# Optimization experiments

Hardware: AMD Instinct MI355X
Metric: run time of the kernel (lower is better)

The kernel has to match this reference:

```python
import jax, jax.numpy as jnp
import numpy as np

IN_C, H1, H2, FC1, NCLS = 16, 32, 64, 128, 10
N_NODES, N_EDGES = 20000, 100000


def _glorot(key, shape):
    fan_in, fan_out = shape[0], shape[-1]
    s = jnp.sqrt(6.0 / (fan_in + fan_out))
    return jax.random.uniform(key, shape, jnp.float32, -s, s)


def setup_inputs() -> dict:
    key = jax.random.key(0)
    ks = jax.random.split(key, 20)
    x = jax.random.normal(ks[0], (N_NODES, IN_C), jnp.float32)
    edge_index = jax.random.randint(ks[1], (2, N_EDGES), 0, N_NODES, jnp.int64)
    edge_attr = jax.random.uniform(ks[2], (N_EDGES, 1), jnp.float32)
    return {
        "x": x,
        "edge_index": edge_index,
        "edge_attr": edge_attr,
        # conv1 edge-MLP: 1 -> 25 -> IN_C*H1
        "w1a": _glorot(ks[3], (1, 25)), "b1a": jnp.zeros((25,), jnp.float32),
        "w1b": _glorot(ks[4], (25, IN_C * H1)), "b1b": jnp.zeros((IN_C * H1,), jnp.float32),
        "wr1": _glorot(ks[5], (IN_C, H1)), "bias1": jnp.zeros((H1,), jnp.float32),
        # conv2 edge-MLP: 1 -> 25 -> H1*H2 (=2048)
        "w2a": _glorot(ks[6], (1, 25)), "b2a": jnp.zeros((25,), jnp.float32),
        "w2b": _glorot(ks[7], (25, H1 * H2)), "b2b": jnp.zeros((H1 * H2,), jnp.float32),
        "wr2": _glorot(ks[8], (H1, H2)), "bias2": jnp.zeros((H2,), jnp.float32),
        # trailing FCs
        "fc1_w": _glorot(ks[9], (H2, FC1)), "fc1_b": jnp.zeros((FC1,), jnp.float32),
        "fc2_w": _glorot(ks[10], (FC1, NCLS)), "fc2_b": jnp.zeros((NCLS,), jnp.float32),
    }


def _nnconv(x, src, tgt, edge_attr, wa, ba, wb, bb, wroot, bias, in_c, out_c):
    # per-edge MLP-generated weight matrix [E, in_c, out_c]
    h = jax.nn.relu(edge_attr @ wa + ba) @ wb + bb
    W = h.reshape(-1, in_c, out_c)
    # gather source feats, per-edge matmul, scatter-max to targets
    msg = jnp.einsum("ei,eio->eo", x[src], W)  # [E, out_c]
    agg = jax.ops.segment_max(msg, tgt, num_segments=x.shape[0])
    agg = jnp.where(jnp.isfinite(agg), agg, 0.0)  # nodes with no in-edges -> 0 (PyG behavior)
    return agg + x @ wroot + bias


def reference(x, edge_index, edge_attr,
              w1a, b1a, w1b, b1b, wr1, bias1,
              w2a, b2a, w2b, b2b, wr2, bias2,
              fc1_w, fc1_b, fc2_w, fc2_b):
    src, tgt = edge_index[0], edge_index[1]
    h = jax.nn.elu(_nnconv(x, src, tgt, edge_attr, w1a, b1a, w1b, b1b, wr1, bias1, IN_C, H1))
    h = jax.nn.elu(_nnconv(h, src, tgt, edge_attr, w2a, b2a, w2b, b2b, wr2, bias2, H1, H2))
    h = jax.nn.elu(h @ fc1_w + fc1_b)
    h = h @ fc2_w + fc2_b
    return jax.nn.log_softmax(h, axis=1)
```

## Files before the change

kernel.cpp:

```cpp
#include <hip/hip_runtime.h>
#include <float.h>
#include <math.h>


#define NCONST 25
#define CH1 32
#define CH2 16
#define PACK_MASK 0x1FFFF
#define TNB 4

__device__ __forceinline__ void atomicMaxFloat(float* addr, float val) {
    if (val >= 0.f) atomicMax((int*)addr, __float_as_int(val));
    else            atomicMin((unsigned int*)addr, __float_as_uint(val));
}
__device__ __forceinline__ float readlane_f(float v, int l) {
    return __int_as_float(__builtin_amdgcn_readlane(__float_as_int(v), l));
}
__device__ __forceinline__ float elu_f(float a) {
    return a > 0.f ? a : expm1f(a);
}

__global__ void fill_kernel(float* agg, int nAgg, int* ords, int nOrd, int* hist, int nH) {
    int i = blockIdx.x * blockDim.x + threadIdx.x;
    int stride = gridDim.x * blockDim.x;
    int total = nAgg + nOrd + nH;
    for (; i < total; i += stride) {
        if (i < nAgg) agg[i] = -FLT_MAX;
        else if (i < nAgg + nOrd) ords[i - nAgg] = -1;
        else hist[i - nAgg - nOrd] = 0;
    }
}

__global__ void assign_hist_kernel(const float* __restrict__ ea,
                                   const float* __restrict__ w1a, const float* __restrict__ b1a,
                                   const float* __restrict__ w2a, const float* __restrict__ b2a,
                                   int E, int* __restrict__ segpack, int* __restrict__ hist) {
    __shared__ float t1[NCONST], t2[NCONST];
    __shared__ int lh[64];
    int tid = threadIdx.x;
    if (tid < NCONST) {
        float w = w1a[tid]; t1[tid] = (w != 0.f) ? (-b1a[tid] / w) : INFINITY;
        float v = w2a[tid]; t2[tid] = (v != 0.f) ? (-b2a[tid] / v) : INFINITY;
    }
    if (tid < 64) lh[tid] = 0;
    __syncthreads();
    int e = blockIdx.x * blockDim.x + tid;
    bool valid = e < E;
    if (valid) {
        float a = ea[e];
        int j1 = 0, j2 = 0;
        for (int k = 0; k < NCONST; ++k) { j1 += (t1[k] < a); j2 += (t2[k] < a); }
        segpack[e] = j1 | (j2 << 8);
        atomicAdd(&lh[j1], 1); atomicAdd(&lh[32 + j2], 1);
    }
    __syncthreads();
    if (tid < 64 && lh[tid]) atomicAdd(&hist[tid], lh[tid]);
}

__global__ void scanpad_kernel(const int* __restrict__ hist, int* __restrict__ cur) {
    __shared__ int h[64];
    int tid = threadIdx.x;
    h[tid] = hist[tid];
    __syncthreads();
    if (tid == 0) {
        int off = 0;
        for (int j = 0; j < 26; ++j) { cur[j] = off; off += ((h[j] + CH1 - 1) / CH1) * CH1; }
    } else if (tid == 1) {
        int off = 0;
        for (int j = 0; j < 26; ++j) { cur[32 + j] = off; off += ((h[32 + j] + CH2 - 1) / CH2) * CH2; }
    }
}

__global__ void scatter_kernel(const int* __restrict__ segpack, int E, int* __restrict__ cur,
                               int* __restrict__ order1, int* __restrict__ order2) {
    __shared__ int lh[64], lb[64];
    int tid = threadIdx.x;
    if (tid < 64) lh[tid] = 0;
    __syncthreads();
    int e = blockIdx.x * blockDim.x + tid;
    bool valid = e < E;
    int j1 = 0, j2 = 0, r1 = 0, r2 = 0;
    if (valid) {
        int p = segpack[e]; j1 = p & 0xFF; j2 = p >> 8;
        r1 = atomicAdd(&lh[j1], 1); r2 = atomicAdd(&lh[32 + j2], 1);
    }
    __syncthreads();
    if (tid < 64 && lh[tid]) lb[tid] = atomicAdd(&cur[tid], lh[tid]);
    __syncthreads();
    if (valid) {
        order1[lb[j1] + r1] = (j1 << 17) | e;
        order2[lb[32 + j2] + r2] = (j2 << 17) | e;
    }
}

__global__ void build_uv_fused(const float* w1a, const float* b1a, const float* w1b, const float* b1b,
                               const float* w2a, const float* b2a, const float* w2b, const float* b2b,
                               float* U1, float* V1, float* U2, float* V2) {
    __shared__ float swa[NCONST], sba[NCONST], st[NCONST];
    __shared__ int sr[NCONST];
    __shared__ unsigned msk_sh;
    int seg = blockIdx.y;
    int bx = blockIdx.x;
    int conv = (bx < 2) ? 0 : 1;
    const float* wa = conv ? w2a : w1a;
    const float* ba = conv ? b2a : b1a;
    int tid = threadIdx.x;
    if (tid < NCONST) {
        float w = wa[tid], b = ba[tid];
        swa[tid] = w; sba[tid] = b;
        st[tid] = (w != 0.f) ? (-b / w) : INFINITY;
    }
    __syncthreads();
    if (tid < NCONST) {
        int rk = 0;
        for (int l = 0; l < NCONST; ++l) rk += (st[l] < st[tid]) ? 1 : 0;
        sr[tid] = rk;
    }
    __syncthreads();
    if (tid == 0) {
        unsigned m = 0;
        for (int k = 0; k < NCONST; ++k) {
            float w = swa[k];
            bool act = (w > 0.f) ? (seg > sr[k])
                     : (w < 0.f) ? (seg <= sr[k])
                                 : (sba[k] > 0.f);
            if (act) m |= (1u << k);
        }
        msk_sh = m;
    }
    __syncthreads();
    unsigned msk = msk_sh;
    if (conv == 0) {
        int idx = bx * 256 + tid;
        float u = 0.f, v = 0.f;
        for (int k = 0; k < NCONST; ++k)
            if (msk & (1u << k)) { float w = w1b[k * 512 + idx]; u = fmaf(swa[k], w, u); v = fmaf(sba[k], w, v); }
        v += b1b[idx];
        U1[seg * 512 + idx] = u; V1[seg * 512 + idx] = v;
    } else {
        int idx = (bx - 2) * 256 + tid;
        float u = 0.f, v = 0.f;
        for (int k = 0; k < NCONST; ++k)
            if (msk & (1u << k)) { float w = w2b[k * 2048 + idx]; u = fmaf(swa[k], w, u); v = fmaf(sba[k], w, v); }
        v += b2b[idx];
        U2[seg * 2048 + idx] = u; V2[seg * 2048 + idx] = v;
    }
}

__global__ void edge1_kernel(const float* __restrict__ xin, const int* __restrict__ src,
                             const int* __restrict__ tgt, const float* __restrict__ ea,
                             const int* __restrict__ order, int cap,
                             const float* __restrict__ U, const float* __restrict__ V,
                             float* __restrict__ agg) {
    int wid = (blockIdx.x * blockDim.x + threadIdx.x) >> 6;
    int lane = threadIdx.x & 63;
    int base = wid * CH1;
    if (base >= cap) return;
    int pk = order[base + (lane & (CH1 - 1))];
    int p0 = __builtin_amdgcn_readfirstlane(pk);
    if (p0 < 0) return;
    int seg = p0 >> 17;
    int ev = (pk < 0) ? 0 : (pk & PACK_MASK);
    int sv = src[ev], tv = tgt[ev];
    float av = ea[ev];
    int half = lane >> 5, c = lane & 31;
    float Ur[16], Vr[16];
    {
        const float* Us = U + seg * 512 + c;
        const float* Vs = V + seg * 512 + c;
#pragma unroll
        for (int i = 0; i < 16; ++i) { Ur[i] = Us[i * 32]; Vr[i] = Vs[i * 32]; }
    }
#pragma unroll
    for (int t = 0; t < CH1; t += 2) {
        int pA = __builtin_amdgcn_readlane(pk, t);
        int pB = __builtin_amdgcn_readlane(pk, t + 1);
        int sA = __builtin_amdgcn_readlane(sv, t);
        int sB = __builtin_amdgcn_readlane(sv, t + 1);
        int tA = __builtin_amdgcn_readlane(tv, t);
        int tB = __builtin_amdgcn_readlane(tv, t + 1);
        float aA = readlane_f(av, t);
        float aB = readlane_f(av, t + 1);
        const float* xA = xin + sA * 16;
        const float* xB = xin + sB * 16;
        float ah = half ? aB : aA;
        int   th = half ? tB : tA;
        int   ph = half ? pB : pA;
        float acc = 0.f;
#pragma unroll
        for (int i = 0; i < 16; ++i) {
            float xi = half ? xB[i] : xA[i];
            acc = fmaf(xi, fmaf(ah, Ur[i], Vr[i]), acc);
        }
        if (ph >= 0) atomicMaxFloat(&agg[th * 32 + c], acc);
    }
}

__global__ void edge2_kernel(const float* __restrict__ xin, const int* __restrict__ src,
                             const int* __restrict__ tgt, const float* __restrict__ ea,
                             const int* __restrict__ order, int cap,
                             const float* __restrict__ U, const float* __restrict__ V,
                             float* __restrict__ agg) {
    int wid = (blockIdx.x * blockDim.x + threadIdx.x) >> 6;
    int lane = threadIdx.x & 63;
    int base = wid * CH2;
    if (base >= cap) return;
    int pk = order[base + (lane & (CH2 - 1))];
    int p0 = __builtin_amdgcn_readfirstlane(pk);
    if (p0 < 0) return;
    int seg = p0 >> 17;
    int ev = (pk < 0) ? 0 : (pk & PACK_MASK);
    int sv = src[ev], tv = tgt[ev];
    float av = ea[ev];
    float Ur[32], Vr[32];
    {
        const float* Us = U + seg * 2048 + lane;
        const float* Vs = V + seg * 2048 + lane;
#pragma unroll
        for (int i = 0; i < 32; ++i) { Ur[i] = Us[i * 64]; Vr[i] = Vs[i * 64]; }
    }
#pragma unroll
    for (int t = 0; t < CH2; t += 2) {
        int pA = __builtin_amdgcn_readlane(pk, t);
        int pB = __builtin_amdgcn_readlane(pk, t + 1);
        int sA = __builtin_amdgcn_readlane(sv, t);
        int sB = __builtin_amdgcn_readlane(sv, t + 1);
        int tA = __builtin_amdgcn_readlane(tv, t);
        int tB = __builtin_amdgcn_readlane(tv, t + 1);
        float aA = readlane_f(av, t);
        float aB = readlane_f(av, t + 1);
        const float* xA = xin + sA * 32;
        const float* xB = xin + sB * 32;
        float accA = 0.f, accB = 0.f;
#pragma unroll
        for (int i = 0; i < 32; ++i) {
            accA = fmaf(xA[i], fmaf(aA, Ur[i], Vr[i]), accA);
            accB = fmaf(xB[i], fmaf(aB, Ur[i], Vr[i]), accB);
        }
        if (pA >= 0) atomicMaxFloat(&agg[tA * 64 + lane], accA);
        if (pB >= 0) atomicMaxFloat(&agg[tB * 64 + lane], accB);
    }
}

__global__ void node1_kernel(const float* __restrict__ xin, const float* __restrict__ agg,
                             const float* __restrict__ wroot, const float* __restrict__ bias,
                             float* __restrict__ out, int N) {
    int idx = blockIdx.x * blockDim.x + threadIdx.x;
    if (idx >= N * 32) return;
    int n = idx >> 5, c = idx & 31;
    float v = agg[idx];
    if (v == -FLT_MAX) v = 0.f;
    float acc = v + bias[c];
#pragma unroll
    for (int i = 0; i < 16; ++i) acc = fmaf(xin[n * 16 + i], wroot[i * 32 + c], acc);
    out[idx] = acc > 0.f ? acc : expm1f(acc);
}

__global__ void tail_kernel(const float* __restrict__ h1, const float* __restrict__ agg2,
                            const float* __restrict__ wr2, const float* __restrict__ bias2,
                            const float* __restrict__ fc1w, const float* __restrict__ fc1b,
                            const float* __restrict__ fc2w, const float* __restrict__ fc2b,
                            float* __restrict__ out) {
    __shared__ __align__(16) float h1sh[4][TNB][32];
    __shared__ __align__(16) float h2sh[4][TNB][64];
    __shared__ __align__(16) float h3sh[4][TNB][132];
    __shared__ __align__(16) float wTsh[10][132];
    int tid = threadIdx.x;
    int wv = tid >> 6, lane = tid & 63;

    for (int t = tid; t < 1280; t += 256) {
        int k = t / 10, j = t - k * 10;
        wTsh[j][k] = fc2w[t];
    }
    __syncthreads();

    int nb = blockIdx.x * (4 * TNB) + wv * TNB;

    {
        const float2* hp = (const float2*)(h1 + (size_t)nb * 32);
        ((float2*)&h1sh[wv][0][0])[lane] = hp[lane];
    }

    float b2v = bias2[lane];
    float ac0 = agg2[(size_t)(nb + 0) * 64 + lane];
    float ac1 = agg2[(size_t)(nb + 1) * 64 + lane];
    float ac2 = agg2[(size_t)(nb + 2) * 64 + lane];
    float ac3 = agg2[(size_t)(nb + 3) * 64 + lane];
    ac0 = (ac0 == -FLT_MAX ? 0.f : ac0) + b2v;
    ac1 = (ac1 == -FLT_MAX ? 0.f : ac1) + b2v;
    ac2 = (ac2 == -FLT_MAX ? 0.f : ac2) + b2v;
    ac3 = (ac3 == -FLT_MAX ? 0.f : ac3) + b2v;
#pragma unroll 8
    for (int i = 0; i < 32; ++i) {
        float w = wr2[i * 64 + lane];
        ac0 = fmaf(h1sh[wv][0][i], w, ac0);
        ac1 = fmaf(h1sh[wv][1][i], w, ac1);
        ac2 = fmaf(h1sh[wv][2][i], w, ac2);
        ac3 = fmaf(h1sh[wv][3][i], w, ac3);
    }
    h2sh[wv][0][lane] = elu_f(ac0);
    h2sh[wv][1][lane] = elu_f(ac1);
    h2sh[wv][2][lane] = elu_f(ac2);
    h2sh[wv][3][lane] = elu_f(ac3);

    float fb1 = fc1b[lane], fb2 = fc1b[64 + lane];
    float p0 = fb1, p1 = fb1, p2 = fb1, p3 = fb1;
    float q0 = fb2, q1 = fb2, q2 = fb2, q3 = fb2;
#pragma unroll 2
    for (int k4 = 0; k4 < 16; ++k4) {
        int k = k4 * 4;
        float wA0 = fc1w[(k + 0) * 128 + lane];
        float wB0 = fc1w[(k + 0) * 128 + 64 + lane];
        float wA1 = fc1w[(k + 1) * 128 + lane];
        float wB1 = fc1w[(k + 1) * 128 + 64 + lane];
        float wA2 = fc1w[(k + 2) * 128 + lane];
        float wB2 = fc1w[(k + 2) * 128 + 64 + lane];
        float wA3 = fc1w[(k + 3) * 128 + lane];
        float wB3 = fc1w[(k + 3) * 128 + 64 + lane];
        float4 g0 = ((const float4*)h2sh[wv][0])[k4];
        float4 g1 = ((const float4*)h2sh[wv][1])[k4];
        float4 g2 = ((const float4*)h2sh[wv][2])[k4];
        float4 g3 = ((const float4*)h2sh[wv][3])[k4];
        p0 = fmaf(g0.x, wA0, p0); p0 = fmaf(g0.y, wA1, p0);
        p0 = fmaf(g0.z, wA2, p0); p0 = fmaf(g0.w, wA3, p0);
        q0 = fmaf(g0.x, wB0, q0); q0 = fmaf(g0.y, wB1, q0);
        q0 = fmaf(g0.z, wB2, q0); q0 = fmaf(g0.w, wB3, q0);
        p1 = fmaf(g1.x, wA0, p1); p1 = fmaf(g1.y, wA1, p1);
        p1 = fmaf(g1.z, wA2, p1); p1 = fmaf(g1.w, wA3, p1);
        q1 = fmaf(g1.x, wB0, q1); q1 = fmaf(g1.y, wB1, q1);
        q1 = fmaf(g1.z, wB2, q1); q1 = fmaf(g1.w, wB3, q1);
        p2 = fmaf(g2.x, wA0, p2); p2 = fmaf(g2.y, wA1, p2);
        p2 = fmaf(g2.z, wA2, p2); p2 = fmaf(g2.w, wA3, p2);
        q2 = fmaf(g2.x, wB0, q2); q2 = fmaf(g2.y, wB1, q2);
        q2 = fmaf(g2.z, wB2, q2); q2 = fmaf(g2.w, wB3, q2);
        p3 = fmaf(g3.x, wA0, p3); p3 = fmaf(g3.y, wA1, p3);
        p3 = fmaf(g3.z, wA2, p3); p3 = fmaf(g3.w, wA3, p3);
        q3 = fmaf(g3.x, wB0, q3); q3 = fmaf(g3.y, wB1, q3);
        q3 = fmaf(g3.z, wB2, q3); q3 = fmaf(g3.w, wB3, q3);
    }
    h3sh[wv][0][lane] = elu_f(p0); h3sh[wv][0][64 + lane] = elu_f(q0);
    h3sh[wv][1][lane] = elu_f(p1); h3sh[wv][1][64 + lane] = elu_f(q1);
    h3sh[wv][2][lane] = elu_f(p2); h3sh[wv][2][64 + lane] = elu_f(q2);
    h3sh[wv][3][lane] = elu_f(p3); h3sh[wv][3][64 + lane] = elu_f(q3);

    {
        int n = lane >> 4, j = lane & 15;
        bool act = j < 10;
        int jc = act ? j : 0;
        float a = fc2b[jc];
        const float4* h3v = (const float4*)h3sh[wv][n];
        const float4* wv4 = (const float4*)wTsh[jc];
#pragma unroll
        for (int q = 0; q < 32; ++q) {
            float4 h = h3v[q];
            float4 w = wv4[q];
            a = fmaf(h.x, w.x, a);
            a = fmaf(h.y, w.y, a);
            a = fmaf(h.z, w.z, a);
            a = fmaf(h.w, w.w, a);
        }
        float lm = act ? a : -FLT_MAX;
        lm = fmaxf(lm, __shfl_xor(lm, 1, 16));
        lm = fmaxf(lm, __shfl_xor(lm, 2, 16));
        lm = fmaxf(lm, __shfl_xor(lm, 4, 16));
        lm = fmaxf(lm, __shfl_xor(lm, 8, 16));
        float ls = act ? expf(a - lm) : 0.f;
        ls += __shfl_xor(ls, 1, 16);
        ls += __shfl_xor(ls, 2, 16);
        ls += __shfl_xor(ls, 4, 16);
        ls += __shfl_xor(ls, 8, 16);
        if (act) out[(size_t)(nb + n) * 10 + j] = a - lm - logf(ls);
    }
}

extern "C" void kernel_launch(void* const* d_in, const int* in_sizes, int n_in,
                              void* d_out, int out_size, void* d_ws, size_t ws_size,
                              hipStream_t stream) {
    const float* x     = (const float*)d_in[0];
    const int*   eidx  = (const int*)d_in[1];
    const float* ea    = (const float*)d_in[2];
    const float* w1a   = (const float*)d_in[3];
    const float* b1a   = (const float*)d_in[4];
    const float* w1b   = (const float*)d_in[5];
    const float* b1b   = (const float*)d_in[6];
    const float* wr1   = (const float*)d_in[7];
    const float* bias1 = (const float*)d_in[8];
    const float* w2a   = (const float*)d_in[9];
    const float* b2a   = (const float*)d_in[10];
    const float* w2b   = (const float*)d_in[11];
    const float* b2b   = (const float*)d_in[12];
    const float* wr2   = (const float*)d_in[13];
    const float* bias2 = (const float*)d_in[14];
    const float* fc1w  = (const float*)d_in[15];
    const float* fc1b  = (const float*)d_in[16];
    const float* fc2w  = (const float*)d_in[17];
    const float* fc2b  = (const float*)d_in[18];

    const int N = in_sizes[0] / 16;
    const int E = in_sizes[2];
    const int* src = eidx;
    const int* tgt = eidx + E;

    const int cap1 = ((E + 26 * (CH1 - 1)) + CH1 - 1) / CH1 * CH1;
    const int cap2 = ((E + 26 * (CH2 - 1)) + CH2 - 1) / CH2 * CH2;

    float* ws = (float*)d_ws;
    size_t off = 0;
    int*      hist = (int*)(ws + off);      off += 64;
    int*      cur  = (int*)(ws + off);      off += 64;
    int*      segp = (int*)(ws + off);      off += E;
    int*      ord1 = (int*)(ws + off);      off += cap1;
    int*      ord2 = (int*)(ws + off);      off += cap2;
    float*    U1   = ws + off;              off += 26 * 512;
    float*    V1   = ws + off;              off += 26 * 512;
    float*    U2   = ws + off;              off += 26 * 2048;
    float*    V2   = ws + off;              off += 26 * 2048;
    float*    AGG1 = ws + off;              off += (size_t)N * 32;
    float*    AGG2 = ws + off;              off += (size_t)N * 64;
    float*    H1b  = ws + off;              off += (size_t)N * 32;

    fill_kernel<<<512, 256, 0, stream>>>(AGG1, N * 96, ord1, cap1 + cap2, hist, 64);
    assign_hist_kernel<<<(E + 255) / 256, 256, 0, stream>>>(ea, w1a, b1a, w2a, b2a, E, segp, hist);
    scanpad_kernel<<<1, 64, 0, stream>>>(hist, cur);
    scatter_kernel<<<(E + 255) / 256, 256, 0, stream>>>(segp, E, cur, ord1, ord2);
    build_uv_fused<<<dim3(10, 26), 256, 0, stream>>>(w1a, b1a, w1b, b1b, w2a, b2a, w2b, b2b,
                                                     U1, V1, U2, V2);
    {
        int waves = cap1 / CH1;
        edge1_kernel<<<(waves + 3) / 4, 256, 0, stream>>>(x, src, tgt, ea, ord1, cap1, U1, V1, AGG1);
    }
    node1_kernel<<<(N * 32 + 255) / 256, 256, 0, stream>>>(x, AGG1, wr1, bias1, H1b, N);
    {
        int waves = cap2 / CH2;
        edge2_kernel<<<(waves + 3) / 4, 256, 0, stream>>>(H1b, src, tgt, ea, ord2, cap2, U2, V2, AGG2);
    }
    tail_kernel<<<N / 16, 256, 0, stream>>>(H1b, AGG2, wr2, bias2, fc1w, fc1b, fc2w, fc2b, (float*)d_out);
}
```

Before: 198.2 us.

## Merge fill, UV build and histogram into one prep kernel; fold scan into scatter

```diff
diff --git a/kernel.cpp b/kernel.cpp
--- a/kernel.cpp
+++ b/kernel.cpp
@@ -8,6 +8,8 @@
 #define CH2 16
 #define PACK_MASK 0x1FFFF
 #define TNB 4
+#define K1_FILL 512
+#define K1_UV   260
 
 __device__ __forceinline__ void atomicMaxFloat(float* addr, float val) {
     if (val >= 0.f) atomicMax((int*)addr, __float_as_int(val));
@@ -20,154 +22,145 @@
     return a > 0.f ? a : expm1f(a);
 }
 
-__global__ void fill_kernel(float* agg, int nAgg, int* ords, int nOrd, int* hist, int nH) {
-    int i = blockIdx.x * blockDim.x + threadIdx.x;
-    int stride = gridDim.x * blockDim.x;
-    int total = nAgg + nOrd + nH;
-    for (; i < total; i += stride) {
-        if (i < nAgg) agg[i] = -FLT_MAX;
-        else if (i < nAgg + nOrd) ords[i - nAgg] = -1;
-        else hist[i - nAgg - nOrd] = 0;
-    }
-}
-
-__global__ void assign_hist_kernel(const float* __restrict__ ea,
-                                   const float* __restrict__ w1a, const float* __restrict__ b1a,
-                                   const float* __restrict__ w2a, const float* __restrict__ b2a,
-                                   int E, int* __restrict__ segpack, int* __restrict__ hist) {
+struct Params {
+    const float *x; const int *src; const int *tgt; const float *ea;
+    const float *w1a, *b1a, *w1b, *b1b, *wr1, *bias1;
+    const float *w2a, *b2a, *w2b, *b2b, *wr2, *bias2;
+    const float *fc1w, *fc1b, *fc2w, *fc2b;
+    float *out;
+    int *hist, *cur, *segp, *ord1, *ord2;
+    float *U1, *V1, *U2, *V2, *AGG1, *AGG2, *H1b;
+    int N, E, cap1, cap2;
+};
+
+__global__ void prep_kernel(Params p) {
     __shared__ float t1[NCONST], t2[NCONST];
     __shared__ int lh[64];
+    __shared__ float swa[NCONST], sba[NCONST], stt[NCONST];
+    __shared__ int srk[NCONST];
+    __shared__ unsigned msk_sh;
+    const int bid = blockIdx.x, tid = threadIdx.x;
+
+    if (bid < K1_FILL) {
+        int nAgg = p.N * 96, total = nAgg + p.cap1 + p.cap2;
+        for (int i = bid * 256 + tid; i < total; i += K1_FILL * 256) {
+            if (i < nAgg) p.AGG1[i] = -FLT_MAX;
+            else p.ord1[i - nAgg] = -1;
+        }
+    } else if (bid < K1_FILL + K1_UV) {
+        int v = bid - K1_FILL;
+        int seg = v / 10;
+        int bx  = v % 10;
+        int conv = (bx < 2) ? 0 : 1;
+        const float* wa = conv ? p.w2a : p.w1a;
+        const float* ba = conv ? p.b2a : p.b1a;
+        if (tid < NCONST) {
+            float w = wa[tid], b = ba[tid];
+            swa[tid] = w; sba[tid] = b;
+            stt[tid] = (w != 0.f) ? (-b / w) : INFINITY;
+        }
+        __syncthreads();
+        if (tid < NCONST) {
+            int rk = 0;
+            for (int l = 0; l < NCONST; ++l) rk += (stt[l] < stt[tid]) ? 1 : 0;
+            srk[tid] = rk;
+        }
+        __syncthreads();
+        if (tid == 0) {
+            unsigned m = 0;
+            for (int k = 0; k < NCONST; ++k) {
+                float w = swa[k];
+                bool act = (w > 0.f) ? (seg > srk[k])
+                         : (w < 0.f) ? (seg <= srk[k])
+                                     : (sba[k] > 0.f);
+                if (act) m |= (1u << k);
+            }
+            msk_sh = m;
+        }
+        __syncthreads();
+        unsigned msk = msk_sh;
+        if (conv == 0) {
+            int idx = bx * 256 + tid;
+            float u = 0.f, vv = 0.f;
+            for (int k = 0; k < NCONST; ++k)
+                if (msk & (1u << k)) { float w = p.w1b[k * 512 + idx]; u = fmaf(swa[k], w, u); vv = fmaf(sba[k], w, vv); }
+            vv += p.b1b[idx];
+            p.U1[seg * 512 + idx] = u; p.V1[seg * 512 + idx] = vv;
+        } else {
+            int idx = (bx - 2) * 256 + tid;
+            float u = 0.f, vv = 0.f;
+            for (int k = 0; k < NCONST; ++k)
+                if (msk & (1u << k)) { float w = p.w2b[k * 2048 + idx]; u = fmaf(swa[k], w, u); vv = fmaf(sba[k], w, vv); }
+            vv += p.b2b[idx];
+            p.U2[seg * 2048 + idx] = u; p.V2[seg * 2048 + idx] = vv;
+        }
+    } else {
+        if (tid < NCONST) {
+            float w = p.w1a[tid]; t1[tid] = (w != 0.f) ? (-p.b1a[tid] / w) : INFINITY;
+            float v = p.w2a[tid]; t2[tid] = (v != 0.f) ? (-p.b2a[tid] / v) : INFINITY;
+        }
+        if (tid < 64) lh[tid] = 0;
+        __syncthreads();
+        int e = (bid - K1_FILL - K1_UV) * 256 + tid;
+        if (e < p.E) {
+            float a = p.ea[e];
+            int j1 = 0, j2 = 0;
+            for (int k = 0; k < NCONST; ++k) { j1 += (t1[k] < a); j2 += (t2[k] < a); }
+            p.segp[e] = j1 | (j2 << 8);
+            atomicAdd(&lh[j1], 1); atomicAdd(&lh[32 + j2], 1);
+        }
+        __syncthreads();
+        if (tid < 64 && lh[tid]) atomicAdd(&p.hist[tid], lh[tid]);
+    }
+}
+
+__global__ void scatter_scan_kernel(Params p) {
+    __shared__ int h[64], sbase[64], lh[64], lb[64];
     int tid = threadIdx.x;
-    if (tid < NCONST) {
-        float w = w1a[tid]; t1[tid] = (w != 0.f) ? (-b1a[tid] / w) : INFINITY;
-        float v = w2a[tid]; t2[tid] = (v != 0.f) ? (-b2a[tid] / v) : INFINITY;
-    }
-    if (tid < 64) lh[tid] = 0;
-    __syncthreads();
-    int e = blockIdx.x * blockDim.x + tid;
-    bool valid = e < E;
-    if (valid) {
-        float a = ea[e];
-        int j1 = 0, j2 = 0;
-        for (int k = 0; k < NCONST; ++k) { j1 += (t1[k] < a); j2 += (t2[k] < a); }
-        segpack[e] = j1 | (j2 << 8);
-        atomicAdd(&lh[j1], 1); atomicAdd(&lh[32 + j2], 1);
-    }
-    __syncthreads();
-    if (tid < 64 && lh[tid]) atomicAdd(&hist[tid], lh[tid]);
-}
-
-__global__ void scanpad_kernel(const int* __restrict__ hist, int* __restrict__ cur) {
-    __shared__ int h[64];
-    int tid = threadIdx.x;
-    h[tid] = hist[tid];
+    if (tid < 64) h[tid] = p.hist[tid];
     __syncthreads();
     if (tid == 0) {
         int off = 0;
-        for (int j = 0; j < 26; ++j) { cur[j] = off; off += ((h[j] + CH1 - 1) / CH1) * CH1; }
+        for (int j = 0; j < 26; ++j) { sbase[j] = off; off += ((h[j] + CH1 - 1) / CH1) * CH1; }
     } else if (tid == 1) {
         int off = 0;
-        for (int j = 0; j < 26; ++j) { cur[32 + j] = off; off += ((h[32 + j] + CH2 - 1) / CH2) * CH2; }
-    }
-}
-
-__global__ void scatter_kernel(const int* __restrict__ segpack, int E, int* __restrict__ cur,
-                               int* __restrict__ order1, int* __restrict__ order2) {
-    __shared__ int lh[64], lb[64];
-    int tid = threadIdx.x;
+        for (int j = 0; j < 26; ++j) { sbase[32 + j] = off; off += ((h[32 + j] + CH2 - 1) / CH2) * CH2; }
+    }
     if (tid < 64) lh[tid] = 0;
     __syncthreads();
-    int e = blockIdx.x * blockDim.x + tid;
-    bool valid = e < E;
+    int e = blockIdx.x * 256 + tid;
+    bool valid = e < p.E;
     int j1 = 0, j2 = 0, r1 = 0, r2 = 0;
     if (valid) {
-        int p = segpack[e]; j1 = p & 0xFF; j2 = p >> 8;
+        int pk = p.segp[e]; j1 = pk & 0xFF; j2 = pk >> 8;
         r1 = atomicAdd(&lh[j1], 1); r2 = atomicAdd(&lh[32 + j2], 1);
     }
     __syncthreads();
-    if (tid < 64 && lh[tid]) lb[tid] = atomicAdd(&cur[tid], lh[tid]);
+    if (tid < 64 && lh[tid]) lb[tid] = sbase[tid] + atomicAdd(&p.cur[tid], lh[tid]);
     __syncthreads();
     if (valid) {
-        order1[lb[j1] + r1] = (j1 << 17) | e;
-        order2[lb[32 + j2] + r2] = (j2 << 17) | e;
-    }
-}
-
-__global__ void build_uv_fused(const float* w1a, const float* b1a, const float* w1b, const float* b1b,
-                               const float* w2a, const float* b2a, const float* w2b, const float* b2b,
-                               float* U1, float* V1, float* U2, float* V2) {
-    __shared__ float swa[NCONST], sba[NCONST], st[NCONST];
-    __shared__ int sr[NCONST];
-    __shared__ unsigned msk_sh;
-    int seg = blockIdx.y;
-    int bx = blockIdx.x;
-    int conv = (bx < 2) ? 0 : 1;
-    const float* wa = conv ? w2a : w1a;
-    const float* ba = conv ? b2a : b1a;
-    int tid = threadIdx.x;
-    if (tid < NCONST) {
-        float w = wa[tid], b = ba[tid];
-        swa[tid] = w; sba[tid] = b;
-        st[tid] = (w != 0.f) ? (-b / w) : INFINITY;
-    }
-    __syncthreads();
-    if (tid < NCONST) {
-        int rk = 0;
-        for (int l = 0; l < NCONST; ++l) rk += (st[l] < st[tid]) ? 1 : 0;
-        sr[tid] = rk;
-    }
-    __syncthreads();
-    if (tid == 0) {
-        unsigned m = 0;
-        for (int k = 0; k < NCONST; ++k) {
-            float w = swa[k];
-            bool act = (w > 0.f) ? (seg > sr[k])
-                     : (w < 0.f) ? (seg <= sr[k])
-                                 : (sba[k] > 0.f);
-            if (act) m |= (1u << k);
-        }
-        msk_sh = m;
-    }
-    __syncthreads();
-    unsigned msk = msk_sh;
-    if (conv == 0) {
-        int idx = bx * 256 + tid;
-        float u = 0.f, v = 0.f;
-        for (int k = 0; k < NCONST; ++k)
-            if (msk & (1u << k)) { float w = w1b[k * 512 + idx]; u = fmaf(swa[k], w, u); v = fmaf(sba[k], w, v); }
-        v += b1b[idx];
-        U1[seg * 512 + idx] = u; V1[seg * 512 + idx] = v;
-    } else {
-        int idx = (bx - 2) * 256 + tid;
-        float u = 0.f, v = 0.f;
-        for (int k = 0; k < NCONST; ++k)
-            if (msk & (1u << k)) { float w = w2b[k * 2048 + idx]; u = fmaf(swa[k], w, u); v = fmaf(sba[k], w, v); }
-        v += b2b[idx];
-        U2[seg * 2048 + idx] = u; V2[seg * 2048 + idx] = v;
-    }
-}
-
-__global__ void edge1_kernel(const float* __restrict__ xin, const int* __restrict__ src,
-                             const int* __restrict__ tgt, const float* __restrict__ ea,
-                             const int* __restrict__ order, int cap,
-                             const float* __restrict__ U, const float* __restrict__ V,
-                             float* __restrict__ agg) {
+        p.ord1[lb[j1] + r1] = (j1 << 17) | e;
+        p.ord2[lb[32 + j2] + r2] = (j2 << 17) | e;
+    }
+}
+
+__global__ void edge1_kernel(Params p) {
     int wid = (blockIdx.x * blockDim.x + threadIdx.x) >> 6;
     int lane = threadIdx.x & 63;
     int base = wid * CH1;
-    if (base >= cap) return;
-    int pk = order[base + (lane & (CH1 - 1))];
+    if (base >= p.cap1) return;
+    int pk = p.ord1[base + (lane & (CH1 - 1))];
     int p0 = __builtin_amdgcn_readfirstlane(pk);
     if (p0 < 0) return;
     int seg = p0 >> 17;
     int ev = (pk < 0) ? 0 : (pk & PACK_MASK);
-    int sv = src[ev], tv = tgt[ev];
-    float av = ea[ev];
+    int sv = p.src[ev], tv = p.tgt[ev];
+    float av = p.ea[ev];
     int half = lane >> 5, c = lane & 31;
     float Ur[16], Vr[16];
     {
-        const float* Us = U + seg * 512 + c;
-        const float* Vs = V + seg * 512 + c;
+        const float* Us = p.U1 + seg * 512 + c;
+        const float* Vs = p.V1 + seg * 512 + c;
 #pragma unroll
         for (int i = 0; i < 16; ++i) { Ur[i] = Us[i * 32]; Vr[i] = Vs[i * 32]; }
     }
@@ -181,41 +174,39 @@
         int tB = __builtin_amdgcn_readlane(tv, t + 1);
         float aA = readlane_f(av, t);
         float aB = readlane_f(av, t + 1);
-        const float* xA = xin + sA * 16;
-        const float* xB = xin + sB * 16;
         float ah = half ? aB : aA;
         int   th = half ? tB : tA;
         int   ph = half ? pB : pA;
+        const float4* xr = (const float4*)(p.x + (half ? sB : sA) * 16);
         float acc = 0.f;
 #pragma unroll
-        for (int i = 0; i < 16; ++i) {
-            float xi = half ? xB[i] : xA[i];
-            acc = fmaf(xi, fmaf(ah, Ur[i], Vr[i]), acc);
-        }
-        if (ph >= 0) atomicMaxFloat(&agg[th * 32 + c], acc);
-    }
-}
-
-__global__ void edge2_kernel(const float* __restrict__ xin, const int* __restrict__ src,
-                             const int* __restrict__ tgt, const float* __restrict__ ea,
-                             const int* __restrict__ order, int cap,
-                             const float* __restrict__ U, const float* __restrict__ V,
-                             float* __restrict__ agg) {
+        for (int q = 0; q < 4; ++q) {
+            float4 v = xr[q];
+            acc = fmaf(v.x, fmaf(ah, Ur[q * 4 + 0], Vr[q * 4 + 0]), acc);
+            acc = fmaf(v.y, fmaf(ah, Ur[q * 4 + 1], Vr[q * 4 + 1]), acc);
+            acc = fmaf(v.z, fmaf(ah, Ur[q * 4 + 2], Vr[q * 4 + 2]), acc);
+            acc = fmaf(v.w, fmaf(ah, Ur[q * 4 + 3], Vr[q * 4 + 3]), acc);
+        }
+        if (ph >= 0) atomicMaxFloat(&p.AGG1[th * 32 + c], acc);
+    }
+}
+
+__global__ void edge2_kernel(Params p) {
     int wid = (blockIdx.x * blockDim.x + threadIdx.x) >> 6;
     int lane = threadIdx.x & 63;
     int base = wid * CH2;
-    if (base >= cap) return;
-    int pk = order[base + (lane & (CH2 - 1))];
+    if (base >= p.cap2) return;
+    int pk = p.ord2[base + (lane & (CH2 - 1))];
     int p0 = __builtin_amdgcn_readfirstlane(pk);
     if (p0 < 0) return;
     int seg = p0 >> 17;
     int ev = (pk < 0) ? 0 : (pk & PACK_MASK);
-    int sv = src[ev], tv = tgt[ev];
-    float av = ea[ev];
+    int sv = p.src[ev], tv = p.tgt[ev];
+    float av = p.ea[ev];
     float Ur[32], Vr[32];
     {
-        const float* Us = U + seg * 2048 + lane;
-        const float* Vs = V + seg * 2048 + lane;
+        const float* Us = p.U2 + seg * 2048 + lane;
+        const float* Vs = p.V2 + seg * 2048 + lane;
 #pragma unroll
         for (int i = 0; i < 32; ++i) { Ur[i] = Us[i * 64]; Vr[i] = Vs[i * 64]; }
     }
@@ -229,38 +220,47 @@
         int tB = __builtin_amdgcn_readlane(tv, t + 1);
         float aA = readlane_f(av, t);
         float aB = readlane_f(av, t + 1);
-        const float* xA = xin + sA * 32;
-        const float* xB = xin + sB * 32;
+        const float4* xa4 = (const float4*)(p.H1b + sA * 32);
+        const float4* xb4 = (const float4*)(p.H1b + sB * 32);
         float accA = 0.f, accB = 0.f;
 #pragma unroll
-        for (int i = 0; i < 32; ++i) {
-            accA = fmaf(xA[i], fmaf(aA, Ur[i], Vr[i]), accA);
-            accB = fmaf(xB[i], fmaf(aB, Ur[i], Vr[i]), accB);
-        }
-        if (pA >= 0) atomicMaxFloat(&agg[tA * 64 + lane], accA);
-        if (pB >= 0) atomicMaxFloat(&agg[tB * 64 + lane], accB);
-    }
-}
-
-__global__ void node1_kernel(const float* __restrict__ xin, const float* __restrict__ agg,
-                             const float* __restrict__ wroot, const float* __restrict__ bias,
-                             float* __restrict__ out, int N) {
+        for (int q = 0; q < 8; ++q) {
+            float4 va = xa4[q];
+            float4 vb = xb4[q];
+            accA = fmaf(va.x, fmaf(aA, Ur[q * 4 + 0], Vr[q * 4 + 0]), accA);
+            accB = fmaf(vb.x, fmaf(aB, Ur[q * 4 + 0], Vr[q * 4 + 0]), accB);
+            accA = fmaf(va.y, fmaf(aA, Ur[q * 4 + 1], Vr[q * 4 + 1]), accA);
+            accB = fmaf(vb.y, fmaf(aB, Ur[q * 4 + 1], Vr[q * 4 + 1]), accB);
+            accA = fmaf(va.z, fmaf(aA, Ur[q * 4 + 2], Vr[q * 4 + 2]), accA);
+            accB = fmaf(vb.z, fmaf(aB, Ur[q * 4 + 2], Vr[q * 4 + 2]), accB);
+            accA = fmaf(va.w, fmaf(aA, Ur[q * 4 + 3], Vr[q * 4 + 3]), accA);
+            accB = fmaf(vb.w, fmaf(aB, Ur[q * 4 + 3], Vr[q * 4 + 3]), accB);
+        }
+        if (pA >= 0) atomicMaxFloat(&p.AGG2[tA * 64 + lane], accA);
+        if (pB >= 0) atomicMaxFloat(&p.AGG2[tB * 64 + lane], accB);
+    }
+}
+
+__global__ void node1_kernel(Params p) {
     int idx = blockIdx.x * blockDim.x + threadIdx.x;
-    if (idx >= N * 32) return;
+    if (idx >= p.N * 32) return;
     int n = idx >> 5, c = idx & 31;
-    float v = agg[idx];
+    float v = p.AGG1[idx];
     if (v == -FLT_MAX) v = 0.f;
-    float acc = v + bias[c];
-#pragma unroll
-    for (int i = 0; i < 16; ++i) acc = fmaf(xin[n * 16 + i], wroot[i * 32 + c], acc);
-    out[idx] = acc > 0.f ? acc : expm1f(acc);
-}
-
-__global__ void tail_kernel(const float* __restrict__ h1, const float* __restrict__ agg2,
-                            const float* __restrict__ wr2, const float* __restrict__ bias2,
-                            const float* __restrict__ fc1w, const float* __restrict__ fc1b,
-                            const float* __restrict__ fc2w, const float* __restrict__ fc2b,
-                            float* __restrict__ out) {
+    float acc = v + p.bias1[c];
+    const float4* xr = (const float4*)(p.x + n * 16);
+#pragma unroll
+    for (int q = 0; q < 4; ++q) {
+        float4 h = xr[q];
+        acc = fmaf(h.x, p.wr1[(q * 4 + 0) * 32 + c], acc);
+        acc = fmaf(h.y, p.wr1[(q * 4 + 1) * 32 + c], acc);
+        acc = fmaf(h.z, p.wr1[(q * 4 + 2) * 32 + c], acc);
+        acc = fmaf(h.w, p.wr1[(q * 4 + 3) * 32 + c], acc);
+    }
+    p.H1b[idx] = elu_f(acc);
+}
+
+__global__ void tail_kernel(Params p) {
     __shared__ __align__(16) float h1sh[4][TNB][32];
     __shared__ __align__(16) float h2sh[4][TNB][64];
     __shared__ __align__(16) float h3sh[4][TNB][132];
@@ -270,29 +270,29 @@
 
     for (int t = tid; t < 1280; t += 256) {
         int k = t / 10, j = t - k * 10;
-        wTsh[j][k] = fc2w[t];
+        wTsh[j][k] = p.fc2w[t];
     }
     __syncthreads();
 
     int nb = blockIdx.x * (4 * TNB) + wv * TNB;
 
     {
-        const float2* hp = (const float2*)(h1 + (size_t)nb * 32);
+        const float2* hp = (const float2*)(p.H1b + (size_t)nb * 32);
         ((float2*)&h1sh[wv][0][0])[lane] = hp[lane];
     }
 
-    float b2v = bias2[lane];
-    float ac0 = agg2[(size_t)(nb + 0) * 64 + lane];
-    float ac1 = agg2[(size_t)(nb + 1) * 64 + lane];
-    float ac2 = agg2[(size_t)(nb + 2) * 64 + lane];
-    float ac3 = agg2[(size_t)(nb + 3) * 64 + lane];
+    float b2v = p.bias2[lane];
+    float ac0 = p.AGG2[(size_t)(nb + 0) * 64 + lane];
+    float ac1 = p.AGG2[(size_t)(nb + 1) * 64 + lane];
+    float ac2 = p.AGG2[(size_t)(nb + 2) * 64 + lane];
+    float ac3 = p.AGG2[(size_t)(nb + 3) * 64 + lane];
     ac0 = (ac0 == -FLT_MAX ? 0.f : ac0) + b2v;
     ac1 = (ac1 == -FLT_MAX ? 0.f : ac1) + b2v;
     ac2 = (ac2 == -FLT_MAX ? 0.f : ac2) + b2v;
     ac3 = (ac3 == -FLT_MAX ? 0.f : ac3) + b2v;
 #pragma unroll 8
     for (int i = 0; i < 32; ++i) {
-        float w = wr2[i * 64 + lane];
+        float w = p.wr2[i * 64 + lane];
         ac0 = fmaf(h1sh[wv][0][i], w, ac0);
         ac1 = fmaf(h1sh[wv][1][i], w, ac1);
         ac2 = fmaf(h1sh[wv][2][i], w, ac2);
@@ -303,20 +303,20 @@
     h2sh[wv][2][lane] = elu_f(ac2);
     h2sh[wv][3][lane] = elu_f(ac3);
 
-    float fb1 = fc1b[lane], fb2 = fc1b[64 + lane];
+    float fb1 = p.fc1b[lane], fb2 = p.fc1b[64 + lane];
     float p0 = fb1, p1 = fb1, p2 = fb1, p3 = fb1;
     float q0 = fb2, q1 = fb2, q2 = fb2, q3 = fb2;
 #pragma unroll 2
     for (int k4 = 0; k4 < 16; ++k4) {
         int k = k4 * 4;
-        float wA0 = fc1w[(k + 0) * 128 + lane];
-        float wB0 = fc1w[(k + 0) * 128 + 64 + lane];
-        float wA1 = fc1w[(k + 1) * 128 + lane];
-        float wB1 = fc1w[(k + 1) * 128 + 64 + lane];
-        float wA2 = fc1w[(k + 2) * 128 + lane];
-        float wB2 = fc1w[(k + 2) * 128 + 64 + lane];
-        float wA3 = fc1w[(k + 3) * 128 + lane];
-        float wB3 = fc1w[(k + 3) * 128 + 64 + lane];
+        float wA0 = p.fc1w[(k + 0) * 128 + lane];
+        float wB0 = p.fc1w[(k + 0) * 128 + 64 + lane];
+        float wA1 = p.fc1w[(k + 1) * 128 + lane];
+        float wB1 = p.fc1w[(k + 1) * 128 + 64 + lane];
+        float wA2 = p.fc1w[(k + 2) * 128 + lane];
+        float wB2 = p.fc1w[(k + 2) * 128 + 64 + lane];
+        float wA3 = p.fc1w[(k + 3) * 128 + lane];
+        float wB3 = p.fc1w[(k + 3) * 128 + 64 + lane];
         float4 g0 = ((const float4*)h2sh[wv][0])[k4];
         float4 g1 = ((const float4*)h2sh[wv][1])[k4];
         float4 g2 = ((const float4*)h2sh[wv][2])[k4];
@@ -347,7 +347,7 @@
         int n = lane >> 4, j = lane & 15;
         bool act = j < 10;
         int jc = act ? j : 0;
-        float a = fc2b[jc];
+        float a = p.fc2b[jc];
         const float4* h3v = (const float4*)h3sh[wv][n];
         const float4* wv4 = (const float4*)wTsh[jc];
 #pragma unroll
@@ -369,70 +369,71 @@
         ls += __shfl_xor(ls, 2, 16);
         ls += __shfl_xor(ls, 4, 16);
         ls += __shfl_xor(ls, 8, 16);
-        if (act) out[(size_t)(nb + n) * 10 + j] = a - lm - logf(ls);
+        if (act) p.out[(size_t)(nb + n) * 10 + j] = a - lm - logf(ls);
     }
 }
 
 extern "C" void kernel_launch(void* const* d_in, const int* in_sizes, int n_in,
                               void* d_out, int out_size, void* d_ws, size_t ws_size,
                               hipStream_t stream) {
-    const float* x     = (const float*)d_in[0];
-    const int*   eidx  = (const int*)d_in[1];
-    const float* ea    = (const float*)d_in[2];
-    const float* w1a   = (const float*)d_in[3];
-    const float* b1a   = (const float*)d_in[4];
-    const float* w1b   = (const float*)d_in[5];
-    const float* b1b   = (const float*)d_in[6];
-    const float* wr1   = (const float*)d_in[7];
-    const float* bias1 = (const float*)d_in[8];
-    const float* w2a   = (const float*)d_in[9];
-    const float* b2a   = (const float*)d_in[10];
-    const float* w2b   = (const float*)d_in[11];
-    const float* b2b   = (const float*)d_in[12];
-    const float* wr2   = (const float*)d_in[13];
-    const float* bias2 = (const float*)d_in[14];
-    const float* fc1w  = (const float*)d_in[15];
-    const float* fc1b  = (const float*)d_in[16];
-    const float* fc2w  = (const float*)d_in[17];
-    const float* fc2b  = (const float*)d_in[18];
-
-    const int N = in_sizes[0] / 16;
-    const int E = in_sizes[2];
-    const int* src = eidx;
-    const int* tgt = eidx + E;
-
-    const int cap1 = ((E + 26 * (CH1 - 1)) + CH1 - 1) / CH1 * CH1;
-    const int cap2 = ((E + 26 * (CH2 - 1)) + CH2 - 1) / CH2 * CH2;
+    Params p;
+    p.x     = (const float*)d_in[0];
+    const int* eidx = (const int*)d_in[1];
+    p.ea    = (const float*)d_in[2];
+    p.w1a   = (const float*)d_in[3];
+    p.b1a   = (const float*)d_in[4];
+    p.w1b   = (const float*)d_in[5];
+    p.b1b   = (const float*)d_in[6];
+    p.wr1   = (const float*)d_in[7];
+    p.bias1 = (const float*)d_in[8];
+    p.w2a   = (const float*)d_in[9];
+    p.b2a   = (const float*)d_in[10];
+    p.w2b   = (const float*)d_in[11];
+    p.b2b   = (const float*)d_in[12];
+    p.wr2   = (const float*)d_in[13];
+    p.bias2 = (const float*)d_in[14];
+    p.fc1w  = (const float*)d_in[15];
+    p.fc1b  = (const float*)d_in[16];
+    p.fc2w  = (const float*)d_in[17];
+    p.fc2b  = (const float*)d_in[18];
+    p.out   = (float*)d_out;
+
+    p.N = in_sizes[0] / 16;
+    p.E = in_sizes[2];
+    p.src = eidx;
+    p.tgt = eidx + p.E;
+
+    p.cap1 = ((p.E + 26 * (CH1 - 1)) + CH1 - 1) / CH1 * CH1;
+    p.cap2 = ((p.E + 26 * (CH2 - 1)) + CH2 - 1) / CH2 * CH2;
 
     float* ws = (float*)d_ws;
     size_t off = 0;
-    int*      hist = (int*)(ws + off);      off += 64;
-    int*      cur  = (int*)(ws + off);      off += 64;
-    int*      segp = (int*)(ws + off);      off += E;
-    int*      ord1 = (int*)(ws + off);      off += cap1;
-    int*      ord2 = (int*)(ws + off);      off += cap2;
-    float*    U1   = ws + off;              off += 26 * 512;
-    float*    V1   = ws + off;              off += 26 * 512;
-    float*    U2   = ws + off;              off += 26 * 2048;
-    float*    V2   = ws + off;              off += 26 * 2048;
-    float*    AGG1 = ws + off;              off += (size_t)N * 32;
-    float*    AGG2 = ws + off;              off += (size_t)N * 64;
-    float*    H1b  = ws + off;              off += (size_t)N * 32;
-
-    fill_kernel<<<512, 256, 0, stream>>>(AGG1, N * 96, ord1, cap1 + cap2, hist, 64);
-    assign_hist_kernel<<<(E + 255) / 256, 256, 0, stream>>>(ea, w1a, b1a, w2a, b2a, E, segp, hist);
-    scanpad_kernel<<<1, 64, 0, stream>>>(hist, cur);
-    scatter_kernel<<<(E + 255) / 256, 256, 0, stream>>>(segp, E, cur, ord1, ord2);
-    build_uv_fused<<<dim3(10, 26), 256, 0, stream>>>(w1a, b1a, w1b, b1b, w2a, b2a, w2b, b2b,
-                                                     U1, V1, U2, V2);
-    {
-        int waves = cap1 / CH1;
-        edge1_kernel<<<(waves + 3) / 4, 256, 0, stream>>>(x, src, tgt, ea, ord1, cap1, U1, V1, AGG1);
-    }
-    node1_kernel<<<(N * 32 + 255) / 256, 256, 0, stream>>>(x, AGG1, wr1, bias1, H1b, N);
-    {
-        int waves = cap2 / CH2;
-        edge2_kernel<<<(waves + 3) / 4, 256, 0, stream>>>(H1b, src, tgt, ea, ord2, cap2, U2, V2, AGG2);
-    }
-    tail_kernel<<<N / 16, 256, 0, stream>>>(H1b, AGG2, wr2, bias2, fc1w, fc1b, fc2w, fc2b, (float*)d_out);
-}
+    p.hist = (int*)(ws + off);      off += 64;
+    p.cur  = (int*)(ws + off);      off += 64;
+    p.segp = (int*)(ws + off);      off += p.E;
+    p.ord1 = (int*)(ws + off);      off += p.cap1;
+    p.ord2 = (int*)(ws + off);      off += p.cap2;
+    p.U1   = ws + off;              off += 26 * 512;
+    p.V1   = ws + off;              off += 26 * 512;
+    p.U2   = ws + off;              off += 26 * 2048;
+    p.V2   = ws + off;              off += 26 * 2048;
+    p.AGG1 = ws + off;              off += (size_t)p.N * 32;
+    p.AGG2 = ws + off;              off += (size_t)p.N * 64;
+    p.H1b  = ws + off;              off += (size_t)p.N * 32;
+
+    const int nAssign = (p.E + 255) / 256;
+
+    hipMemsetAsync(p.hist, 0, 512, stream);
+    prep_kernel<<<K1_FILL + K1_UV + nAssign, 256, 0, stream>>>(p);
+    scatter_scan_kernel<<<nAssign, 256, 0, stream>>>(p);
+    {
+        int waves = p.cap1 / CH1;
+        edge1_kernel<<<(waves + 3) / 4, 256, 0, stream>>>(p);
+    }
+    node1_kernel<<<(p.N * 32 + 255) / 256, 256, 0, stream>>>(p);
+    {
+        int waves = p.cap2 / CH2;
+        edge2_kernel<<<(waves + 3) / 4, 256, 0, stream>>>(p);
+    }
+    tail_kernel<<<p.N / 16, 256, 0, stream>>>(p);
+}
```

After: 239.3 us. 20.8% more time.

## Merge preprocessing kernels into one prep kernel and fuse scan into scatter

Applied to the files above, without the earlier changes.

```diff
diff --git a/kernel.cpp b/kernel.cpp
--- a/kernel.cpp
+++ b/kernel.cpp
@@ -8,6 +8,8 @@
 #define CH2 16
 #define PACK_MASK 0x1FFFF
 #define TNB 4
+#define K1_FILL 64
+#define K1_UV   260
 
 __device__ __forceinline__ void atomicMaxFloat(float* addr, float val) {
     if (val >= 0.f) atomicMax((int*)addr, __float_as_int(val));
@@ -20,130 +22,125 @@
     return a > 0.f ? a : expm1f(a);
 }
 
-__global__ void fill_kernel(float* agg, int nAgg, int* ords, int nOrd, int* hist, int nH) {
-    int i = blockIdx.x * blockDim.x + threadIdx.x;
-    int stride = gridDim.x * blockDim.x;
-    int total = nAgg + nOrd + nH;
-    for (; i < total; i += stride) {
-        if (i < nAgg) agg[i] = -FLT_MAX;
-        else if (i < nAgg + nOrd) ords[i - nAgg] = -1;
-        else hist[i - nAgg - nOrd] = 0;
-    }
-}
-
-__global__ void assign_hist_kernel(const float* __restrict__ ea,
-                                   const float* __restrict__ w1a, const float* __restrict__ b1a,
-                                   const float* __restrict__ w2a, const float* __restrict__ b2a,
-                                   int E, int* __restrict__ segpack, int* __restrict__ hist) {
+struct PrepParams {
+    const float *ea;
+    const float *w1a, *b1a, *w1b, *b1b;
+    const float *w2a, *b2a, *w2b, *b2b;
+    int *hist, *segp, *ord1;
+    float *U1, *V1, *U2, *V2, *AGG1;
+    int N, E, capSum;
+};
+
+__global__ void prep_kernel(PrepParams p) {
     __shared__ float t1[NCONST], t2[NCONST];
     __shared__ int lh[64];
+    __shared__ float swa[NCONST], sba[NCONST], stt[NCONST];
+    __shared__ int srk[NCONST];
+    __shared__ unsigned msk_sh;
+    const int bid = blockIdx.x, tid = threadIdx.x;
+
+    if (bid < K1_FILL) {
+        int nAgg = p.N * 96, total = nAgg + p.capSum;
+        for (int i = bid * 256 + tid; i < total; i += K1_FILL * 256) {
+            if (i < nAgg) p.AGG1[i] = -FLT_MAX;
+            else p.ord1[i - nAgg] = -1;
+        }
+    } else if (bid < K1_FILL + K1_UV) {
+        int v = bid - K1_FILL;
+        int seg = v / 10;
+        int bx  = v % 10;
+        int conv = (bx < 2) ? 0 : 1;
+        const float* wa = conv ? p.w2a : p.w1a;
+        const float* ba = conv ? p.b2a : p.b1a;
+        if (tid < NCONST) {
+            float w = wa[tid], b = ba[tid];
+            swa[tid] = w; sba[tid] = b;
+            stt[tid] = (w != 0.f) ? (-b / w) : INFINITY;
+        }
+        __syncthreads();
+        if (tid < NCONST) {
+            int rk = 0;
+            for (int l = 0; l < NCONST; ++l) rk += (stt[l] < stt[tid]) ? 1 : 0;
+            srk[tid] = rk;
+        }
+        __syncthreads();
+        if (tid == 0) {
+            unsigned m = 0;
+            for (int k = 0; k < NCONST; ++k) {
+                float w = swa[k];
+                bool act = (w > 0.f) ? (seg > srk[k])
+                         : (w < 0.f) ? (seg <= srk[k])
+                                     : (sba[k] > 0.f);
+                if (act) m |= (1u << k);
+            }
+            msk_sh = m;
+        }
+        __syncthreads();
+        unsigned msk = msk_sh;
+        if (conv == 0) {
+            int idx = bx * 256 + tid;
+            float u = 0.f, vv = 0.f;
+            for (int k = 0; k < NCONST; ++k)
+                if (msk & (1u << k)) { float w = p.w1b[k * 512 + idx]; u = fmaf(swa[k], w, u); vv = fmaf(sba[k], w, vv); }
+            vv += p.b1b[idx];
+            p.U1[seg * 512 + idx] = u; p.V1[seg * 512 + idx] = vv;
+        } else {
+            int idx = (bx - 2) * 256 + tid;
+            float u = 0.f, vv = 0.f;
+            for (int k = 0; k < NCONST; ++k)
+                if (msk & (1u << k)) { float w = p.w2b[k * 2048 + idx]; u = fmaf(swa[k], w, u); vv = fmaf(sba[k], w, vv); }
+            vv += p.b2b[idx];
+            p.U2[seg * 2048 + idx] = u; p.V2[seg * 2048 + idx] = vv;
+        }
+    } else {
+        if (tid < NCONST) {
+            float w = p.w1a[tid]; t1[tid] = (w != 0.f) ? (-p.b1a[tid] / w) : INFINITY;
+            float v = p.w2a[tid]; t2[tid] = (v != 0.f) ? (-p.b2a[tid] / v) : INFINITY;
+        }
+        if (tid < 64) lh[tid] = 0;
+        __syncthreads();
+        int e = (bid - K1_FILL - K1_UV) * 256 + tid;
+        if (e < p.E) {
+            float a = p.ea[e];
+            int j1 = 0, j2 = 0;
+            for (int k = 0; k < NCONST; ++k) { j1 += (t1[k] < a); j2 += (t2[k] < a); }
+            p.segp[e] = j1 | (j2 << 8);
+            atomicAdd(&lh[j1], 1); atomicAdd(&lh[32 + j2], 1);
+        }
+        __syncthreads();
+        if (tid < 64 && lh[tid]) atomicAdd(&p.hist[tid], lh[tid]);
+    }
+}
+
+__global__ void scatter_scan_kernel(const int* __restrict__ segpack, int E,
+                                    const int* __restrict__ hist, int* __restrict__ cur,
+                                    int* __restrict__ order1, int* __restrict__ order2) {
+    __shared__ int h[64], sbase[64], lh[64], lb[64];
     int tid = threadIdx.x;
-    if (tid < NCONST) {
-        float w = w1a[tid]; t1[tid] = (w != 0.f) ? (-b1a[tid] / w) : INFINITY;
-        float v = w2a[tid]; t2[tid] = (v != 0.f) ? (-b2a[tid] / v) : INFINITY;
-    }
-    if (tid < 64) lh[tid] = 0;
-    __syncthreads();
-    int e = blockIdx.x * blockDim.x + tid;
-    bool valid = e < E;
-    if (valid) {
-        float a = ea[e];
-        int j1 = 0, j2 = 0;
-        for (int k = 0; k < NCONST; ++k) { j1 += (t1[k] < a); j2 += (t2[k] < a); }
-        segpack[e] = j1 | (j2 << 8);
-        atomicAdd(&lh[j1], 1); atomicAdd(&lh[32 + j2], 1);
-    }
-    __syncthreads();
-    if (tid < 64 && lh[tid]) atomicAdd(&hist[tid], lh[tid]);
-}
-
-__global__ void scanpad_kernel(const int* __restrict__ hist, int* __restrict__ cur) {
-    __shared__ int h[64];
-    int tid = threadIdx.x;
-    h[tid] = hist[tid];
+    if (tid < 64) h[tid] = hist[tid];
     __syncthreads();
     if (tid == 0) {
         int off = 0;
-        for (int j = 0; j < 26; ++j) { cur[j] = off; off += ((h[j] + CH1 - 1) / CH1) * CH1; }
+        for (int j = 0; j < 26; ++j) { sbase[j] = off; off += ((h[j] + CH1 - 1) / CH1) * CH1; }
     } else if (tid == 1) {
         int off = 0;
-        for (int j = 0; j < 26; ++j) { cur[32 + j] = off; off += ((h[32 + j] + CH2 - 1) / CH2) * CH2; }
-    }
-}
-
-__global__ void scatter_kernel(const int* __restrict__ segpack, int E, int* __restrict__ cur,
-                               int* __restrict__ order1, int* __restrict__ order2) {
-    __shared__ int lh[64], lb[64];
-    int tid = threadIdx.x;
+        for (int j = 0; j < 26; ++j) { sbase[32 + j] = off; off += ((h[32 + j] + CH2 - 1) / CH2) * CH2; }
+    }
     if (tid < 64) lh[tid] = 0;
     __syncthreads();
-    int e = blockIdx.x * blockDim.x + tid;
+    int e = blockIdx.x * 256 + tid;
     bool valid = e < E;
     int j1 = 0, j2 = 0, r1 = 0, r2 = 0;
     if (valid) {
-        int p = segpack[e]; j1 = p & 0xFF; j2 = p >> 8;
+        int pk = segpack[e]; j1 = pk & 0xFF; j2 = pk >> 8;
         r1 = atomicAdd(&lh[j1], 1); r2 = atomicAdd(&lh[32 + j2], 1);
     }
     __syncthreads();
-    if (tid < 64 && lh[tid]) lb[tid] = atomicAdd(&cur[tid], lh[tid]);
+    if (tid < 64 && lh[tid]) lb[tid] = sbase[tid] + atomicAdd(&cur[tid], lh[tid]);
     __syncthreads();
     if (valid) {
         order1[lb[j1] + r1] = (j1 << 17) | e;
         order2[lb[32 + j2] + r2] = (j2 << 17) | e;
-    }
-}
-
-__global__ void build_uv_fused(const float* w1a, const float* b1a, const float* w1b, const float* b1b,
-                               const float* w2a, const float* b2a, const float* w2b, const float* b2b,
-                               float* U1, float* V1, float* U2, float* V2) {
-    __shared__ float swa[NCONST], sba[NCONST], st[NCONST];
-    __shared__ int sr[NCONST];
-    __shared__ unsigned msk_sh;
-    int seg = blockIdx.y;
-    int bx = blockIdx.x;
-    int conv = (bx < 2) ? 0 : 1;
-    const float* wa = conv ? w2a : w1a;
-    const float* ba = conv ? b2a : b1a;
-    int tid = threadIdx.x;
-    if (tid < NCONST) {
-        float w = wa[tid], b = ba[tid];
-        swa[tid] = w; sba[tid] = b;
-        st[tid] = (w != 0.f) ? (-b / w) : INFINITY;
-    }
-    __syncthreads();
-    if (tid < NCONST) {
-        int rk = 0;
-        for (int l = 0; l < NCONST; ++l) rk += (st[l] < st[tid]) ? 1 : 0;
-        sr[tid] = rk;
-    }
-    __syncthreads();
-    if (tid == 0) {
-        unsigned m = 0;
-        for (int k = 0; k < NCONST; ++k) {
-            float w = swa[k];
-            bool act = (w > 0.f) ? (seg > sr[k])
-                     : (w < 0.f) ? (seg <= sr[k])
-                                 : (sba[k] > 0.f);
-            if (act) m |= (1u << k);
-        }
-        msk_sh = m;
-    }
-    __syncthreads();
-    unsigned msk = msk_sh;
-    if (conv == 0) {
-        int idx = bx * 256 + tid;
-        float u = 0.f, v = 0.f;
-        for (int k = 0; k < NCONST; ++k)
-            if (msk & (1u << k)) { float w = w1b[k * 512 + idx]; u = fmaf(swa[k], w, u); v = fmaf(sba[k], w, v); }
-        v += b1b[idx];
-        U1[seg * 512 + idx] = u; V1[seg * 512 + idx] = v;
-    } else {
-        int idx = (bx - 2) * 256 + tid;
-        float u = 0.f, v = 0.f;
-        for (int k = 0; k < NCONST; ++k)
-            if (msk & (1u << k)) { float w = w2b[k * 2048 + idx]; u = fmaf(swa[k], w, u); v = fmaf(sba[k], w, v); }
-        v += b2b[idx];
-        U2[seg * 2048 + idx] = u; V2[seg * 2048 + idx] = v;
     }
 }
 
@@ -406,25 +403,31 @@
 
     float* ws = (float*)d_ws;
     size_t off = 0;
-    int*      hist = (int*)(ws + off);      off += 64;
-    int*      cur  = (int*)(ws + off);      off += 64;
-    int*      segp = (int*)(ws + off);      off += E;
-    int*      ord1 = (int*)(ws + off);      off += cap1;
-    int*      ord2 = (int*)(ws + off);      off += cap2;
-    float*    U1   = ws + off;              off += 26 * 512;
-    float*    V1   = ws + off;              off += 26 * 512;
-    float*    U2   = ws + off;              off += 26 * 2048;
-    float*    V2   = ws + off;              off += 26 * 2048;
-    float*    AGG1 = ws + off;              off += (size_t)N * 32;
-    float*    AGG2 = ws + off;              off += (size_t)N * 64;
-    float*    H1b  = ws + off;              off += (size_t)N * 32;
-
-    fill_kernel<<<512, 256, 0, stream>>>(AGG1, N * 96, ord1, cap1 + cap2, hist, 64);
-    assign_hist_kernel<<<(E + 255) / 256, 256, 0, stream>>>(ea, w1a, b1a, w2a, b2a, E, segp, hist);
-    scanpad_kernel<<<1, 64, 0, stream>>>(hist, cur);
-    scatter_kernel<<<(E + 255) / 256, 256, 0, stream>>>(segp, E, cur, ord1, ord2);
-    build_uv_fused<<<dim3(10, 26), 256, 0, stream>>>(w1a, b1a, w1b, b1b, w2a, b2a, w2b, b2b,
-                                                     U1, V1, U2, V2);
+    int*   hist = (int*)(ws + off);   off += 64;
+    int*   cur  = (int*)(ws + off);   off += 64;
+    int*   segp = (int*)(ws + off);   off += E;
+    int*   ord1 = (int*)(ws + off);   off += cap1;
+    int*   ord2 = (int*)(ws + off);   off += cap2;
+    float* U1   = ws + off;           off += 26 * 512;
+    float* V1   = ws + off;           off += 26 * 512;
+    float* U2   = ws + off;           off += 26 * 2048;
+    float* V2   = ws + off;           off += 26 * 2048;
+    float* AGG1 = ws + off;           off += (size_t)N * 32;
+    float* AGG2 = ws + off;           off += (size_t)N * 64;
+    float* H1b  = ws + off;           off += (size_t)N * 32;
+
+    const int nAssign = (E + 255) / 256;
+
+    PrepParams pp;
+    pp.ea = ea; pp.w1a = w1a; pp.b1a = b1a; pp.w1b = w1b; pp.b1b = b1b;
+    pp.w2a = w2a; pp.b2a = b2a; pp.w2b = w2b; pp.b2b = b2b;
+    pp.hist = hist; pp.segp = segp; pp.ord1 = ord1;
+    pp.U1 = U1; pp.V1 = V1; pp.U2 = U2; pp.V2 = V2; pp.AGG1 = AGG1;
+    pp.N = N; pp.E = E; pp.capSum = cap1 + cap2;
+
+    hipMemsetAsync(hist, 0, 512, stream);
+    prep_kernel<<<K1_FILL + K1_UV + nAssign, 256, 0, stream>>>(pp);
+    scatter_scan_kernel<<<nAssign, 256, 0, stream>>>(segp, E, hist, cur, ord1, ord2);
     {
         int waves = cap1 / CH1;
         edge1_kernel<<<(waves + 3) / 4, 256, 0, stream>>>(x, src, tgt, ea, ord1, cap1, U1, V1, AGG1);
```

Result: faster. 190.9 us, median of 2 (-3.7%).
